# Kernel tuning notes

Hardware: AMD Instinct MI355X
Metric: run time of the kernel (lower is better)

The kernel has to match this reference:

```python
import jax, jax.numpy as jnp
import numpy as np
from jax import lax

B, S, IN, H = 16, 128, 200, 256


def _lstm_dir(x_tb, Wih, Whh, bih, bhh):
    # x_tb: [S, B, in]; PyTorch LSTM gate order (i, f, g, o)
    h0 = jnp.zeros((x_tb.shape[1], H), x_tb.dtype)

    def step(carry, x_t):
        h, c = carry
        g = x_t @ Wih.T + h @ Whh.T + bih + bhh  # [B, 4H]
        i, f, gg, o = jnp.split(g, 4, axis=-1)
        c = jax.nn.sigmoid(f) * c + jax.nn.sigmoid(i) * jnp.tanh(gg)
        h = jax.nn.sigmoid(o) * jnp.tanh(c)
        return (h, c), h

    _, hs = lax.scan(step, (h0, h0), x_tb)
    return hs  # [S, B, H]


def _bilstm_layer(x, Wih, Whh, bih, bhh):
    # x: [B, S, in]; params stacked over direction axis [2, ...]
    xt = jnp.swapaxes(x, 0, 1)
    f = _lstm_dir(xt, Wih[0], Whh[0], bih[0], bhh[0])
    b = _lstm_dir(xt[::-1], Wih[1], Whh[1], bih[1], bhh[1])[::-1]
    return jnp.swapaxes(jnp.concatenate([f, b], axis=-1), 0, 1)  # [B, S, 2H]


def _forward(sentence, Wih0, Whh0, bih0, bhh0, Wih1, Whh1, bih1, bhh1,
             W1, b1, W2, b2, W3, b3, tree):
    emb = _bilstm_layer(sentence, Wih0, Whh0, bih0, bhh0)  # [B,S,512]
    emb = _bilstm_layer(emb, Wih1, Whh1, bih1, bhh1)       # [B,S,512]
    D = emb.shape[-1]
    # fc1 on concat(emb[v1], emb[v2]) == per-node halves + broadcast add
    Ha = emb @ W1[:, :D].T   # [B,S,256] head part
    Hb = emb @ W1[:, D:].T   # [B,S,256] dependent part
    h1 = jax.nn.relu(Ha[:, :, None, :] + Hb[:, None, :, :] + b1)  # [B,S,S,256]
    h2 = jax.nn.relu(h1 @ W2.T + b2)                               # [B,S,S,128]
    score = jax.nn.relu(jnp.squeeze(h2 @ W3.T + b3, -1))           # [B,S,S]
    v = jnp.arange(S)
    # valid edges: dep >= 1, head != dep (root col 0 and diagonal stay 0)
    mask = (v[None, :] != v[:, None]) & (v[None, :] >= 1)
    score = score * mask[None, :, :]

    heads, deps = tree[:, 1:, 0], tree[:, 1:, 1]  # [B, S-1]
    K = S - 1
    idx = jnp.broadcast_to(deps[:, None, :], (B, S, K))
    cols = jnp.take_along_axis(score, idx, axis=2)     # score[b, j, dep_k]
    excl = v[None, :, None] == deps[:, None, :]        # exclude j == dep
    norm = jnp.sum(jnp.where(excl, 0.0, jnp.exp(cols)), axis=1)  # [B,K]
    num = score[jnp.arange(B)[:, None], heads, deps]             # [B,K]
    loss = jnp.sum(jnp.sum(jnp.log(norm) - num, axis=-1) / (S - 1))
    return loss, score


def setup_inputs() -> dict:
    key = jax.random.key(0)
    ks = jax.random.split(key, 17)
    sc = jnp.float32(0.05)

    def n(k, shape):
        return jax.random.normal(k, shape, jnp.float32) * sc

    return {
        "sentence": jax.random.normal(ks[0], (B, S, IN), jnp.float32),
        "Wih0": n(ks[1], (2, 4 * H, IN)),
        "Whh0": n(ks[2], (2, 4 * H, H)),
        "bih0": n(ks[3], (2, 4 * H)),
        "bhh0": n(ks[4], (2, 4 * H)),
        "Wih1": n(ks[5], (2, 4 * H, 2 * H)),
        "Whh1": n(ks[6], (2, 4 * H, H)),
        "bih1": n(ks[7], (2, 4 * H)),
        "bhh1": n(ks[8], (2, 4 * H)),
        "W1": n(ks[9], (256, 1024)),
        "b1": n(ks[10], (256,)),
        "W2": n(ks[11], (128, 256)),
        "b2": n(ks[12], (128,)),
        "W3": n(ks[13], (1, 128)),
        "b3": n(ks[14], (1,)),
        "real_dependency_tree": jax.random.randint(ks[15], (B, S, 2), 0, S, jnp.int32),
        "real_seq_len": jnp.full((B,), S, jnp.int32),
    }


def reference(sentence, Wih0, Whh0, bih0, bhh0, Wih1, Whh1, bih1, bhh1,
              W1, b1, W2, b2, W3, b3, real_dependency_tree, real_seq_len):
    # all sentences are full length S (real_seq_len == S), so shapes are static
    del real_seq_len
    return _forward(sentence, Wih0, Whh0, bih0, bhh0, Wih1, Whh1, bih1, bhh1,
                    W1, b1, W2, b2, W3, b3, real_dependency_tree)
```

## Files before the change

kernel.cpp:

```cpp
#include <hip/hip_runtime.h>
#include <hip/hip_bf16.h>
#include <cstdint>
#include <cstddef>


typedef __attribute__((ext_vector_type(8))) short bf16x8;
typedef __attribute__((ext_vector_type(4))) float f32x4;
typedef __attribute__((ext_vector_type(4))) unsigned short u16x4;

__device__ __forceinline__ float bf2f(unsigned short u) {
    return __uint_as_float(((unsigned)u) << 16);
}
__device__ __forceinline__ unsigned short f2bf(float f) {
    unsigned u = __float_as_uint(f);
    u = (u + 0x7FFFu + ((u >> 16) & 1u)) >> 16;
    return (unsigned short)u;
}

__device__ __forceinline__ unsigned f2e4m3(float f) {
    unsigned u = __float_as_uint(f);
    unsigned s = (u >> 24) & 0x80u;
    int expf_ = (int)((u >> 23) & 0xFF);
    if (expf_ == 0) return s;
    int exp = expf_ - 127;
    if (exp < -10) return s;
    unsigned M = (u & 0x7FFFFF) | 0x800000;
    int e8 = exp + 7;
    int shift = 20;
    if (e8 < 1) { shift = 21 - e8; e8 = 0; }
    unsigned q = M >> shift;
    unsigned rem = M & ((1u << shift) - 1u);
    unsigned half = 1u << (shift - 1);
    if (rem > half || (rem == half && (q & 1))) q++;
    if (q >= 16) { q >>= 1; e8++; }
    if (e8 == 0 && (q & 8)) e8 = 1;
    if (e8 >= 16 || (e8 == 15 && (q & 7) == 7)) return s | 0x7Eu;
    return s | ((unsigned)e8 << 4) | (q & 7u);
}


__global__ void k_transpose_N1024(const float* __restrict__ src, float* __restrict__ dst, int K) {
    int z = blockIdx.z;
    int idx = blockIdx.x * 256 + threadIdx.x;
    if (idx >= K * 1024) return;
    int k = idx >> 10, n = idx & 1023;
    dst[(size_t)z * K * 1024 + idx] = src[(size_t)z * 1024 * K + (size_t)n * K + k];
}

__global__ void k_wfrag8(const float* __restrict__ Whh, unsigned char* __restrict__ Wfrag8) {
    int idx = blockIdx.x * 256 + threadIdx.x;
    int l = idx & 63;
    int t = (idx >> 6) & 3;
    int ks = (idx >> 8) & 7;
    int w = (idx >> 11) & 15;
    int d = idx >> 15;
    int r = l & 15;
    int kbase = ks * 32 + (l >> 4) * 8;
    int row = (r & 3) * 256 + w * 16 + t * 4 + (r >> 2);
    const float* src = Whh + (size_t)d * (1024 * 256) + (size_t)row * 256 + kbase;
    unsigned char* dst = Wfrag8 + (size_t)idx * 8;
#pragma unroll
    for (int e = 0; e < 8; ++e) {
        int c = (e & 1) * 4 + (e >> 1);
        dst[e] = (unsigned char)f2e4m3(64.f * src[c]);
    }
}

__global__ void k_w2frag(const float* __restrict__ W2, unsigned short* __restrict__ w2f) {
    int idx = blockIdx.x * 256 + threadIdx.x;
    if (idx >= 4096) return;
    int l = idx & 63;
    int ks = (idx >> 6) & 7;
    int nt = idx >> 9;
    const float* src = W2 + (size_t)(nt * 16 + (l & 15)) * 256 + ks * 32 + (l >> 4) * 8;
    unsigned short* dst = w2f + (size_t)idx * 8;
#pragma unroll
    for (int e = 0; e < 8; ++e) dst[e] = f2bf(src[e]);
}

__global__ void k_w1t(const float* __restrict__ W1, float* __restrict__ dst) {
    int idx = blockIdx.x * 256 + threadIdx.x;
    if (idx >= 512 * 512) return;
    int k = idx >> 9, o = idx & 511;
    dst[idx] = (o < 256) ? W1[(size_t)o * 1024 + k] : W1[(size_t)(o - 256) * 1024 + 512 + k];
}

__global__ void k_bias(const float* __restrict__ bih0, const float* __restrict__ bhh0,
                       const float* __restrict__ bih1, const float* __restrict__ bhh1,
                       const float* __restrict__ b1,
                       float* __restrict__ bsum0, float* __restrict__ bsum1, float* __restrict__ bhab) {
    int idx = blockIdx.x * 256 + threadIdx.x;
    if (idx < 2048) bsum0[idx] = bih0[idx] + bhh0[idx];
    else if (idx < 4096) { int i = idx - 2048; bsum1[i] = bih1[i] + bhh1[i]; }
    else if (idx < 4608) { int i = idx - 4096; bhab[i] = (i < 256) ? b1[i] : 0.f; }
}

__global__ __launch_bounds__(256) void k_reorder(const float* __restrict__ xg, float* __restrict__ xgf) {
    int idx = blockIdx.x * 256 + threadIdx.x;
    int n4 = idx & 255;
    int m = (idx >> 8) & 2047;
    int d = idx >> 19;
    int n0 = n4 * 4;
    int q = n0 >> 8;
    int jbase = n0 & 255;
    int b = m >> 7, t = m & 127;
    float4 v = *(const float4*)(xg + ((size_t)(d * 2048 + m)) * 1024 + n0);
    float* base = xgf + (size_t)d * 2097152;
    float vv[4] = {v.x * 64.f, v.y * 64.f, v.z * 64.f, v.w * 64.f};
#pragma unroll
    for (int dj = 0; dj < 4; ++dj) {
        int j = jbase + dj;
        int fi = (t * 4096 + (j >> 4) * 256 + ((j >> 2) & 3) * 64 + dj * 16 + b) * 4 + q;
        base[fi] = vv[dj];
    }
}

__global__ __launch_bounds__(256) void k_gemm(
    const float* __restrict__ A, const float* __restrict__ Wt,
    const float* __restrict__ bias, float* __restrict__ out,
    int M, int K, int N)
{
    int z = blockIdx.z;
    const float* Wtz = Wt + (size_t)z * K * N;
    float* outz = out + (size_t)z * M * N;
    const float* biasz = bias + (size_t)z * N;

    __shared__ float As[16 * 512];
    int tid = threadIdx.x;
    int mq = tid >> 6;
    int nq = tid & 63;
    int n0 = blockIdx.x * 256 + nq * 4;
    int mbase = blockIdx.y * 16;

    for (int r = 0; r < 16; ++r) {
        const float* Ar = A + (size_t)(mbase + r) * K;
        for (int c = tid; c < K; c += 256) As[r * K + c] = Ar[c];
    }
    __syncthreads();

    float4 bv = *(const float4*)(biasz + n0);
    float acc[4][4];
#pragma unroll
    for (int mi = 0; mi < 4; mi++) { acc[mi][0] = bv.x; acc[mi][1] = bv.y; acc[mi][2] = bv.z; acc[mi][3] = bv.w; }

    const float* asr = As + (mq * 4) * K;
    for (int k = 0; k < K; ++k) {
        float4 w = *(const float4*)(Wtz + (size_t)k * N + n0);
        float x0 = asr[k];
        float x1 = asr[K + k];
        float x2 = asr[2 * K + k];
        float x3 = asr[3 * K + k];
        acc[0][0] += x0 * w.x; acc[0][1] += x0 * w.y; acc[0][2] += x0 * w.z; acc[0][3] += x0 * w.w;
        acc[1][0] += x1 * w.x; acc[1][1] += x1 * w.y; acc[1][2] += x1 * w.z; acc[1][3] += x1 * w.w;
        acc[2][0] += x2 * w.x; acc[2][1] += x2 * w.y; acc[2][2] += x2 * w.z; acc[2][3] += x2 * w.w;
        acc[3][0] += x3 * w.x; acc[3][1] += x3 * w.y; acc[3][2] += x3 * w.z; acc[3][3] += x3 * w.w;
    }
#pragma unroll
    for (int mi = 0; mi < 4; mi++) {
        size_t m = (size_t)mbase + mq * 4 + mi;
        *(float4*)(outz + m * N + n0) = make_float4(acc[mi][0], acc[mi][1], acc[mi][2], acc[mi][3]);
    }
}

__global__ __launch_bounds__(256) void k_gemm_tl(
    const unsigned short* __restrict__ embt, const float* __restrict__ Wt,
    const float* __restrict__ bias, float* __restrict__ out,
    int K, int N)
{
    int z = blockIdx.z;
    const float* Wtz = Wt + (size_t)z * K * N;
    float* outz = out + (size_t)z * 2048 * N;
    const float* biasz = bias + (size_t)z * N;

    __shared__ float As[16 * 512];
    int tid = threadIdx.x;
    int mq = tid >> 6;
    int nq = tid & 63;
    int n0 = blockIdx.x * 256 + nq * 4;
    int mbase = blockIdx.y * 16;
    int bb = mbase >> 7;
    int tt0 = mbase & 127;

    for (int r = 0; r < 16; ++r) {
        const unsigned short* Ar = embt + (size_t)(tt0 + r) * 8192 + bb;
        for (int c = tid; c < K; c += 256) As[r * K + c] = bf2f(Ar[c * 16]);
    }
    __syncthreads();

    float4 bv = *(const float4*)(biasz + n0);
    float acc[4][4];
#pragma unroll
    for (int mi = 0; mi < 4; mi++) { acc[mi][0] = bv.x; acc[mi][1] = bv.y; acc[mi][2] = bv.z; acc[mi][3] = bv.w; }

    const float* asr = As + (mq * 4) * K;
    for (int k = 0; k < K; ++k) {
        float4 w = *(const float4*)(Wtz + (size_t)k * N + n0);
        float x0 = asr[k];
        float x1 = asr[K + k];
        float x2 = asr[2 * K + k];
        float x3 = asr[3 * K + k];
        acc[0][0] += x0 * w.x; acc[0][1] += x0 * w.y; acc[0][2] += x0 * w.z; acc[0][3] += x0 * w.w;
        acc[1][0] += x1 * w.x; acc[1][1] += x1 * w.y; acc[1][2] += x1 * w.z; acc[1][3] += x1 * w.w;
        acc[2][0] += x2 * w.x; acc[2][1] += x2 * w.y; acc[2][2] += x2 * w.z; acc[2][3] += x2 * w.w;
        acc[3][0] += x3 * w.x; acc[3][1] += x3 * w.y; acc[3][2] += x3 * w.z; acc[3][3] += x3 * w.w;
    }
#pragma unroll
    for (int mi = 0; mi < 4; mi++) {
        size_t m = (size_t)mbase + mq * 4 + mi;
        *(float4*)(outz + m * N + n0) = make_float4(acc[mi][0], acc[mi][1], acc[mi][2], acc[mi][3]);
    }
}

#define GATE8(A, C, H) { \
    float gi = A[0] * 0.015625f, gf = A[1] * 0.015625f, gg = A[2] * 0.015625f, go = A[3] * 0.015625f; \
    float si = __builtin_amdgcn_rcpf(1.f + __expf(-gi)); \
    float sf = __builtin_amdgcn_rcpf(1.f + __expf(-gf)); \
    float so = __builtin_amdgcn_rcpf(1.f + __expf(-go)); \
    float eg = __expf(2.f * gg); \
    float tg = 1.f - 2.f * __builtin_amdgcn_rcpf(eg + 1.f); \
    C = sf * C + si * tg; \
    float ec = __expf(2.f * C); \
    float tc = 1.f - 2.f * __builtin_amdgcn_rcpf(ec + 1.f); \
    H = so * tc; }

__global__ __launch_bounds__(1024) void k_lstm_mfma(
    const float* __restrict__ xgf,
    const unsigned char* __restrict__ Wfrag8,
    unsigned short* __restrict__ embt)
{
    const int d = blockIdx.x;
    const int tid = threadIdx.x;
    const int w = tid >> 6;
    const int l = tid & 63;
    const int b = l & 15;
    const int jh = l >> 4;

    __shared__ __align__(16) unsigned char Wlds[131072];
    __shared__ __align__(8) unsigned char hB[4096];

    {
        const uint4* wsrc = (const uint4*)(Wfrag8 + (size_t)d * 262144);
        uint4* wdst = (uint4*)Wlds;
        for (int i = tid; i < 8192; i += 1024) wdst[i] = wsrc[i];
    }
    ((unsigned*)hB)[tid] = 0u;

    const int sgn = d ? -1 : 1;
    int t = d ? 127 : 0;
    const f32x4* xb = (const f32x4*)(xgf) + (size_t)d * 524288;
    const int xo = w * 256 + l;

    f32x4 a0 = xb[t * 4096 + xo];
    f32x4 a1 = xb[t * 4096 + xo + 64];
    f32x4 a2 = xb[t * 4096 + xo + 128];
    f32x4 a3 = xb[t * 4096 + xo + 192];

    float c0 = 0.f, c1 = 0.f, c2 = 0.f, c3 = 0.f;
    const int hrd = jh * 128 + b * 8;
    const unsigned char* Wp = Wlds + (size_t)w * 16384 + (size_t)l * 8;
    unsigned short* embp = embt + (size_t)d * 4096 + (size_t)w * 256 + l;
    unsigned char* hw = hB + w * 256 + b * 8 + jh * 2;
    __syncthreads();

    for (int s = 0; s < 128; ++s) {
#pragma unroll
        for (int ks = 0; ks < 8; ++ks) {
            long hf = *(const long*)(hB + ks * 512 + hrd);
            long w0 = *(const long*)(Wp + (ks * 4 + 0) * 512);
            long w1 = *(const long*)(Wp + (ks * 4 + 1) * 512);
            long w2 = *(const long*)(Wp + (ks * 4 + 2) * 512);
            long w3 = *(const long*)(Wp + (ks * 4 + 3) * 512);
            a0 = __builtin_amdgcn_mfma_f32_16x16x32_fp8_fp8(w0, hf, a0, 0, 0, 0);
            a1 = __builtin_amdgcn_mfma_f32_16x16x32_fp8_fp8(w1, hf, a1, 0, 0, 0);
            a2 = __builtin_amdgcn_mfma_f32_16x16x32_fp8_fp8(w2, hf, a2, 0, 0, 0);
            a3 = __builtin_amdgcn_mfma_f32_16x16x32_fp8_fp8(w3, hf, a3, 0, 0, 0);
        }

        float h0, h1, h2, h3;
        GATE8(a0, c0, h0);
        GATE8(a1, c1, h1);
        GATE8(a2, c2, h2);
        GATE8(a3, c3, h3);

        unsigned r01, r23;
        asm("v_cvt_pk_bf16_f32 %0, %1, %2" : "=v"(r01) : "v"(h0), "v"(h1));
        asm("v_cvt_pk_bf16_f32 %0, %1, %2" : "=v"(r23) : "v"(h2), "v"(h3));
        {
            unsigned short* p0 = embp + (size_t)t * 8192;
            p0[0]   = (unsigned short)r01;
            p0[64]  = (unsigned short)(r01 >> 16);
            p0[128] = (unsigned short)r23;
            p0[192] = (unsigned short)(r23 >> 16);
        }

        unsigned q01 = __builtin_amdgcn_cvt_pk_fp8_f32(h0, h1, 0, false);
        unsigned q23 = __builtin_amdgcn_cvt_pk_fp8_f32(h2, h3, 0, false);

        int tn = (s == 127) ? t : (t + sgn);
        a0 = xb[tn * 4096 + xo];
        a1 = xb[tn * 4096 + xo + 64];
        a2 = xb[tn * 4096 + xo + 128];
        a3 = xb[tn * 4096 + xo + 192];
        __syncthreads();
        *(unsigned short*)(hw)       = (unsigned short)q01;
        *(unsigned short*)(hw + 128) = (unsigned short)q23;
        __syncthreads();
        t = tn;
    }
}

__global__ __launch_bounds__(256, 2) void k_scorer_mfma(
    const float* __restrict__ HaHb, const unsigned short* __restrict__ w2f,
    const float* __restrict__ b2, const float* __restrict__ W3,
    const float* __restrict__ b3v, float* __restrict__ score)
{
    const int jt = blockIdx.x, it = blockIdx.y, b = blockIdx.z;
    const int j0 = jt * 16, i0 = it * 16;
    const int tid = threadIdx.x;
    const int w = tid >> 6;
    const int l = tid & 63;
    const int n_l = l & 15;
    const int kq = l >> 4;

    __shared__ __align__(16) unsigned short HaS[16 * 264];
    __shared__ __align__(16) unsigned short HbS[16 * 264];

    {
        const float* base = HaHb + ((size_t)(b * 128)) * 512;
        int rr = tid >> 4;
        int q = tid & 15;
#pragma unroll
        for (int rep = 0; rep < 4; ++rep) {
            int k0 = q * 4 + rep * 64;
            float4 va = *(const float4*)(base + (size_t)(i0 + rr) * 512 + k0);
            float4 vb = *(const float4*)(base + (size_t)(j0 + rr) * 512 + 256 + k0);
            u16x4 ua = { f2bf(va.x), f2bf(va.y), f2bf(va.z), f2bf(va.w) };
            u16x4 ub = { f2bf(vb.x), f2bf(vb.y), f2bf(vb.z), f2bf(vb.w) };
            *(u16x4*)(&HaS[rr * 264 + k0]) = ua;
            *(u16x4*)(&HbS[rr * 264 + k0]) = ub;
        }
    }

    float b2v[8], w3v[8];
#pragma unroll
    for (int nt = 0; nt < 8; ++nt) {
        b2v[nt] = b2[nt * 16 + n_l];
        w3v[nt] = W3[nt * 16 + n_l];
    }

    f32x4 acc[4][8];
#pragma unroll
    for (int il = 0; il < 4; ++il)
#pragma unroll
        for (int nt = 0; nt < 8; ++nt) acc[il][nt] = f32x4{0.f, 0.f, 0.f, 0.f};

    const bf16x8* wbase = (const bf16x8*)w2f;
    bf16x8 wf[8], wfn[8];
#pragma unroll
    for (int nt = 0; nt < 8; ++nt) wf[nt] = wbase[(nt * 8 + 0) * 64 + l];

    __syncthreads();

#pragma unroll
    for (int ks = 0; ks < 8; ++ks) {
        if (ks < 7) {
#pragma unroll
            for (int nt = 0; nt < 8; ++nt) wfn[nt] = wbase[(nt * 8 + ks + 1) * 64 + l];
        }
#pragma unroll
        for (int il = 0; il < 4; ++il) {
            const int irow = w * 4 + il;
            bf16x8 ha = *(const bf16x8*)(&HaS[irow * 264 + ks * 32 + kq * 8]);
            bf16x8 hb = *(const bf16x8*)(&HbS[n_l * 264 + ks * 32 + kq * 8]);
            bf16x8 av;
#pragma unroll
            for (int e = 0; e < 8; ++e) {
                float v = bf2f((unsigned short)ha[e]) + bf2f((unsigned short)hb[e]);
                v = v > 0.f ? v : 0.f;
                av[e] = (short)f2bf(v);
            }
#pragma unroll
            for (int nt = 0; nt < 8; ++nt)
                acc[il][nt] = __builtin_amdgcn_mfma_f32_16x16x32_bf16(av, wf[nt], acc[il][nt], 0, 0, 0);
        }
#pragma unroll
        for (int nt = 0; nt < 8; ++nt) wf[nt] = wfn[nt];
    }

    const float bb3 = b3v[0];
#pragma unroll
    for (int il = 0; il < 4; ++il) {
        float p[4];
#pragma unroll
        for (int reg = 0; reg < 4; ++reg) {
            float v = 0.f;
#pragma unroll
            for (int nt = 0; nt < 8; ++nt) {
                float h2v = acc[il][nt][reg] + b2v[nt];
                h2v = h2v > 0.f ? h2v : 0.f;
                v += h2v * w3v[nt];
            }
            p[reg] = v;
        }
#pragma unroll
        for (int m = 1; m < 16; m <<= 1) {
            p[0] += __shfl_xor(p[0], m);
            p[1] += __shfl_xor(p[1], m);
            p[2] += __shfl_xor(p[2], m);
            p[3] += __shfl_xor(p[3], m);
        }
        if (n_l == 0) {
            const int i = i0 + w * 4 + il;
            const int jb = j0 + kq * 4;
            float4 sv;
            float* pv = &sv.x;
#pragma unroll
            for (int reg = 0; reg < 4; ++reg) {
                int jg = jb + reg;
                float sc = p[reg] + bb3;
                sc = sc > 0.f ? sc : 0.f;
                if (jg == i || jg == 0) sc = 0.f;
                pv[reg] = sc;
            }
            *(float4*)(&score[((size_t)(b * 128 + i)) * 128 + jb]) = sv;
        }
    }
}

__global__ __launch_bounds__(128) void k_loss1(
    const float* __restrict__ score, const int* __restrict__ tree, float* __restrict__ res)
{
    int k = blockIdx.x;
    int b = blockIdx.y;
    int head = tree[((size_t)b * 128 + k + 1) * 2 + 0];
    int dep  = tree[((size_t)b * 128 + k + 1) * 2 + 1];
    int i = threadIdx.x;
    float s = score[((size_t)b * 128 + i) * 128 + dep];
    float v = (i == dep) ? 0.f : __expf(s);
    __shared__ float redu[2];
#pragma unroll
    for (int off = 32; off >= 1; off >>= 1) v += __shfl_down(v, off, 64);
    if ((i & 63) == 0) redu[i >> 6] = v;
    __syncthreads();
    if (i == 0) {
        float norm = redu[0] + redu[1];
        float num = score[((size_t)b * 128 + head) * 128 + dep];
        res[b * 127 + k] = __logf(norm) - num;
    }
}

__global__ __launch_bounds__(256) void k_loss2(const float* __restrict__ res, float* __restrict__ out) {
    int tid = threadIdx.x;
    float a = 0.f;
    for (int idx = tid; idx < 16 * 127; idx += 256) a += res[idx];
    __shared__ float sm[256];
    sm[tid] = a;
    __syncthreads();
    for (int off = 128; off >= 1; off >>= 1) {
        if (tid < off) sm[tid] += sm[tid + off];
        __syncthreads();
    }
    if (tid == 0) out[0] = sm[0] / 127.f;
}

extern "C" void kernel_launch(void* const* d_in, const int* in_sizes, int n_in,
                              void* d_out, int out_size, void* d_ws, size_t ws_size,
                              hipStream_t stream) {
    (void)in_sizes; (void)n_in; (void)out_size; (void)ws_size;
    const float* X    = (const float*)d_in[0];
    const float* Wih0 = (const float*)d_in[1];
    const float* Whh0 = (const float*)d_in[2];
    const float* bih0 = (const float*)d_in[3];
    const float* bhh0 = (const float*)d_in[4];
    const float* Wih1 = (const float*)d_in[5];
    const float* Whh1 = (const float*)d_in[6];
    const float* bih1 = (const float*)d_in[7];
    const float* bhh1 = (const float*)d_in[8];
    const float* W1   = (const float*)d_in[9];
    const float* b1   = (const float*)d_in[10];
    const float* W2   = (const float*)d_in[11];
    const float* b2   = (const float*)d_in[12];
    const float* W3   = (const float*)d_in[13];
    const float* b3   = (const float*)d_in[14];
    const int*   tree = (const int*)d_in[15];
    float* out = (float*)d_out;

    float* ws = (float*)d_ws;
    size_t o = 0;
    float* WihT0 = ws + o; o += (size_t)2 * 200 * 1024;
    float* WihT1 = ws + o; o += (size_t)2 * 512 * 1024;
    float* W1T   = ws + o; o += (size_t)512 * 512;
    float* bsum0 = ws + o; o += 2048;
    float* bsum1 = ws + o; o += 2048;
    float* bhab  = ws + o; o += 512;
    unsigned char* Wf0 = (unsigned char*)(ws + o); o += (size_t)2 * 16 * 8 * 4 * 64 * 8 / 4;
    unsigned char* Wf1 = (unsigned char*)(ws + o); o += (size_t)2 * 16 * 8 * 4 * 64 * 8 / 4;
    unsigned short* w2f = (unsigned short*)(ws + o); o += (size_t)8 * 8 * 64 * 8 / 2;
    float* xg   = ws + o; o += (size_t)2 * 2048 * 1024;
    float* xgf  = ws + o; o += (size_t)2 * 2048 * 1024;
    unsigned short* embt0 = (unsigned short*)(ws + o); o += (size_t)128 * 512 * 16 / 2;
    unsigned short* embt1 = (unsigned short*)(ws + o); o += (size_t)128 * 512 * 16 / 2;
    float* HaHb = ws + o; o += (size_t)2048 * 512;
    float* res  = ws + o; o += 2048;

    k_transpose_N1024<<<dim3(800, 1, 2), 256, 0, stream>>>(Wih0, WihT0, 200);
    k_transpose_N1024<<<dim3(2048, 1, 2), 256, 0, stream>>>(Wih1, WihT1, 512);
    k_wfrag8<<<256, 256, 0, stream>>>(Whh0, Wf0);
    k_wfrag8<<<256, 256, 0, stream>>>(Whh1, Wf1);
    k_w2frag<<<16, 256, 0, stream>>>(W2, w2f);
    k_w1t<<<1024, 256, 0, stream>>>(W1, W1T);
    k_bias<<<18, 256, 0, stream>>>(bih0, bhh0, bih1, bhh1, b1, bsum0, bsum1, bhab);

    k_gemm<<<dim3(4, 128, 2), 256, 0, stream>>>(X, WihT0, bsum0, xg, 2048, 200, 1024);
    k_reorder<<<4096, 256, 0, stream>>>(xg, xgf);
    k_lstm_mfma<<<2, 1024, 0, stream>>>(xgf, Wf0, embt0);
    k_gemm_tl<<<dim3(4, 128, 2), 256, 0, stream>>>(embt0, WihT1, bsum1, xg, 512, 1024);
    k_reorder<<<4096, 256, 0, stream>>>(xg, xgf);
    k_lstm_mfma<<<2, 1024, 0, stream>>>(xgf, Wf1, embt1);
    k_gemm_tl<<<dim3(2, 128, 1), 256, 0, stream>>>(embt1, W1T, bhab, HaHb, 512, 512);
    k_scorer_mfma<<<dim3(8, 8, 16), 256, 0, stream>>>(HaHb, w2f, b2, W3, b3, out + 1);
    k_loss1<<<dim3(127, 16), 128, 0, stream>>>(out + 1, tree, res);
    k_loss2<<<1, 256, 0, stream>>>(res, out);
}
```

Baseline: 796.2 us.

## Interleave fp8 Whh fragments for 128-bit loads and split weights between LDS and global

The pre-packed fp8 recurrent weight fragments are reordered so each lane's four tile fragments for a k-step are contiguous 32 bytes. The recurrent loop can then fetch them with two 16-byte loads instead of four 8-byte loads. Waves 0-7 read weights from LDS, while waves 8-15 read their weights directly from global memory (L2/L1) each step. This is meant to cut LDS instruction count and bandwidth pressure on the serial LSTM critical path, but the global-reading waves risk higher per-step latency, and the LDS staging may be inconsistent with the new layout.

Result: slower. 1.064 ms (+33.7%).

```diff
diff --git a/kernel.cpp b/kernel.cpp
--- a/kernel.cpp
+++ b/kernel.cpp
@@ -7,6 +7,7 @@
 typedef __attribute__((ext_vector_type(8))) short bf16x8;
 typedef __attribute__((ext_vector_type(4))) float f32x4;
 typedef __attribute__((ext_vector_type(4))) unsigned short u16x4;
+typedef __attribute__((ext_vector_type(2))) long i64x2;
 
 __device__ __forceinline__ float bf2f(unsigned short u) {
     return __uint_as_float(((unsigned)u) << 16);
@@ -49,16 +50,16 @@
 
 __global__ void k_wfrag8(const float* __restrict__ Whh, unsigned char* __restrict__ Wfrag8) {
     int idx = blockIdx.x * 256 + threadIdx.x;
-    int l = idx & 63;
-    int t = (idx >> 6) & 3;
+    int t4 = idx & 3;
+    int l = (idx >> 2) & 63;
     int ks = (idx >> 8) & 7;
     int w = (idx >> 11) & 15;
     int d = idx >> 15;
     int r = l & 15;
     int kbase = ks * 32 + (l >> 4) * 8;
-    int row = (r & 3) * 256 + w * 16 + t * 4 + (r >> 2);
+    int row = (r & 3) * 256 + w * 16 + t4 * 4 + (r >> 2);
     const float* src = Whh + (size_t)d * (1024 * 256) + (size_t)row * 256 + kbase;
-    unsigned char* dst = Wfrag8 + (size_t)idx * 8;
+    unsigned char* dst = Wfrag8 + ((size_t)(((d * 16 + w) * 8 + ks) * 64 + l)) * 32 + t4 * 8;
 #pragma unroll
     for (int e = 0; e < 8; ++e) {
         int c = (e & 1) * 4 + (e >> 1);
@@ -257,23 +258,35 @@
 
     float c0 = 0.f, c1 = 0.f, c2 = 0.f, c3 = 0.f;
     const int hrd = jh * 128 + b * 8;
-    const unsigned char* Wp = Wlds + (size_t)w * 16384 + (size_t)l * 8;
+    const unsigned char* WpL = Wlds + (size_t)w * 16384 + (size_t)l * 32;
+    const unsigned char* WpG = Wfrag8 + (size_t)d * 262144 + (size_t)w * 16384 + (size_t)l * 32;
     unsigned short* embp = embt + (size_t)d * 4096 + (size_t)w * 256 + l;
     unsigned char* hw = hB + w * 256 + b * 8 + jh * 2;
     __syncthreads();
 
     for (int s = 0; s < 128; ++s) {
-#pragma unroll
-        for (int ks = 0; ks < 8; ++ks) {
-            long hf = *(const long*)(hB + ks * 512 + hrd);
-            long w0 = *(const long*)(Wp + (ks * 4 + 0) * 512);
-            long w1 = *(const long*)(Wp + (ks * 4 + 1) * 512);
-            long w2 = *(const long*)(Wp + (ks * 4 + 2) * 512);
-            long w3 = *(const long*)(Wp + (ks * 4 + 3) * 512);
-            a0 = __builtin_amdgcn_mfma_f32_16x16x32_fp8_fp8(w0, hf, a0, 0, 0, 0);
-            a1 = __builtin_amdgcn_mfma_f32_16x16x32_fp8_fp8(w1, hf, a1, 0, 0, 0);
-            a2 = __builtin_amdgcn_mfma_f32_16x16x32_fp8_fp8(w2, hf, a2, 0, 0, 0);
-            a3 = __builtin_amdgcn_mfma_f32_16x16x32_fp8_fp8(w3, hf, a3, 0, 0, 0);
+        if (w < 8) {
+#pragma unroll
+            for (int ks = 0; ks < 8; ++ks) {
+                long hf = *(const long*)(hB + ks * 512 + hrd);
+                i64x2 pa = *(const i64x2*)(WpL + ks * 2048);
+                i64x2 pb = *(const i64x2*)(WpL + ks * 2048 + 16);
+                a0 = __builtin_amdgcn_mfma_f32_16x16x32_fp8_fp8(pa.x, hf, a0, 0, 0, 0);
+                a1 = __builtin_amdgcn_mfma_f32_16x16x32_fp8_fp8(pa.y, hf, a1, 0, 0, 0);
+                a2 = __builtin_amdgcn_mfma_f32_16x16x32_fp8_fp8(pb.x, hf, a2, 0, 0, 0);
+                a3 = __builtin_amdgcn_mfma_f32_16x16x32_fp8_fp8(pb.y, hf, a3, 0, 0, 0);
+            }
+        } else {
+#pragma unroll
+            for (int ks = 0; ks < 8; ++ks) {
+                long hf = *(const long*)(hB + ks * 512 + hrd);
+                i64x2 pa = *(const i64x2*)(WpG + ks * 2048);
+                i64x2 pb = *(const i64x2*)(WpG + ks * 2048 + 16);
+                a0 = __builtin_amdgcn_mfma_f32_16x16x32_fp8_fp8(pa.x, hf, a0, 0, 0, 0);
+                a1 = __builtin_amdgcn_mfma_f32_16x16x32_fp8_fp8(pa.y, hf, a1, 0, 0, 0);
+                a2 = __builtin_amdgcn_mfma_f32_16x16x32_fp8_fp8(pb.x, hf, a2, 0, 0, 0);
+                a3 = __builtin_amdgcn_mfma_f32_16x16x32_fp8_fp8(pb.y, hf, a3, 0, 0, 0);
+            }
         }
 
         float h0, h1, h2, h3;
```

## Split each LSTM direction across two co-located CUs with flag-based h exchange

Applied to the files above, without the earlier changes.

Each LSTM direction now runs on two 512-thread workgroups instead of one 1024-thread workgroup. Sixteen blocks are launched, each reads its XCC id, and pairs that share an XCC are picked so that two pairs do the work while the rest exit. Half of each block's recurrent weights is held in registers and the other half in LDS. Every timestep the two halves of the hidden state are swapped through a global payload buffer using release/acquire flags. This spreads per-step MFMA and LDS traffic over two CUs, but adds an inter-CU round trip through L2 on every step, bounded spin loops that could hang or desync, and two extra memsets.

After: 916.6 us. +15.1%, slower.

```diff
diff --git a/kernel.cpp b/kernel.cpp
--- a/kernel.cpp
+++ b/kernel.cpp
@@ -223,32 +223,89 @@
     float tc = 1.f - 2.f * __builtin_amdgcn_rcpf(ec + 1.f); \
     H = so * tc; }
 
-__global__ __launch_bounds__(1024) void k_lstm_mfma(
+__global__ __launch_bounds__(512, 2) void k_lstm_mfma(
     const float* __restrict__ xgf,
     const unsigned char* __restrict__ Wfrag8,
-    unsigned short* __restrict__ embt)
+    unsigned short* __restrict__ embt,
+    int* ctrl,
+    unsigned char* pay)
 {
-    const int d = blockIdx.x;
+    const int bid = blockIdx.x;
     const int tid = threadIdx.x;
-    const int w = tid >> 6;
+    const int wv = tid >> 6;
     const int l = tid & 63;
     const int b = l & 15;
     const int jh = l >> 4;
 
-    __shared__ __align__(16) unsigned char Wlds[131072];
+    __shared__ __align__(16) unsigned char Wlds[81920];
     __shared__ __align__(8) unsigned char hB[4096];
-
+    __shared__ int role_sh[4];
+
+    if (tid == 0) {
+        unsigned xcc = 0;
+        asm volatile("s_getreg_b32 %0, hwreg(20, 0, 32)" : "=s"(xcc));
+        __hip_atomic_store(&ctrl[1 + bid], (int)(xcc & 7), __ATOMIC_RELAXED, __HIP_MEMORY_SCOPE_AGENT);
+        __hip_atomic_fetch_add(&ctrl[0], 1, __ATOMIC_ACQ_REL, __HIP_MEMORY_SCOPE_AGENT);
+        long it = 0;
+        while (__hip_atomic_load(&ctrl[0], __ATOMIC_ACQUIRE, __HIP_MEMORY_SCOPE_AGENT) < 16 && it < (1 << 24)) {
+            ++it; __builtin_amdgcn_s_sleep(2);
+        }
+        int x[16];
+        for (int i = 0; i < 16; ++i)
+            x[i] = __hip_atomic_load(&ctrl[1 + i], __ATOMIC_RELAXED, __HIP_MEMORY_SCOPE_AGENT) & 7;
+        int pend[8];
+        for (int i = 0; i < 8; ++i) pend[i] = -1;
+        int np = 0, dd = -1, hh = 0;
+        for (int i = 0; i < 16; ++i) {
+            int xc = x[i];
+            if (pend[xc] < 0) pend[xc] = i;
+            else {
+                if (np < 2) {
+                    if (pend[xc] == bid) { dd = np; hh = 0; }
+                    else if (i == bid) { dd = np; hh = 1; }
+                }
+                np++;
+                pend[xc] = -1;
+            }
+        }
+        if (np < 2) {
+            dd = (bid < 4) ? (bid >> 1) : -1;
+            hh = bid & 1;
+        }
+        role_sh[0] = dd; role_sh[1] = hh;
+    }
+    __syncthreads();
+    const int d = role_sh[0];
+    const int hh = role_sh[1];
+    if (d < 0) return;
+
+    const int sg = hh * 8 + wv;
     {
-        const uint4* wsrc = (const uint4*)(Wfrag8 + (size_t)d * 262144);
+        const uint4* wsrc = (const uint4*)(Wfrag8 + (size_t)d * 262144 + (size_t)(hh * 8 + 4) * 16384);
         uint4* wdst = (uint4*)Wlds;
-        for (int i = tid; i < 8192; i += 1024) wdst[i] = wsrc[i];
-    }
-    ((unsigned*)hB)[tid] = 0u;
+        for (int i = tid; i < 4096; i += 512) wdst[i] = wsrc[i];
+    }
+    ((uint64_t*)hB)[tid] = 0ull;
+
+    long W0[8][4];
+    if (wv < 4) {
+        const unsigned char* wg0 = Wfrag8 + ((size_t)(d * 16 + sg)) * 16384;
+#pragma unroll
+        for (int ks = 0; ks < 8; ++ks)
+#pragma unroll
+            for (int t4 = 0; t4 < 4; ++t4)
+                W0[ks][t4] = *(const long*)(wg0 + ((size_t)((ks * 4 + t4) * 64 + l)) * 8);
+#pragma unroll
+        for (int ks = 0; ks < 8; ++ks)
+#pragma unroll
+            for (int t4 = 0; t4 < 4; ++t4)
+                asm volatile("" : "+v"(W0[ks][t4]));
+    }
 
     const int sgn = d ? -1 : 1;
     int t = d ? 127 : 0;
     const f32x4* xb = (const f32x4*)(xgf) + (size_t)d * 524288;
-    const int xo = w * 256 + l;
+    const int xo = sg * 256 + l;
 
     f32x4 a0 = xb[t * 4096 + xo];
     f32x4 a1 = xb[t * 4096 + xo + 64];
@@ -257,23 +314,36 @@
 
     float c0 = 0.f, c1 = 0.f, c2 = 0.f, c3 = 0.f;
     const int hrd = jh * 128 + b * 8;
-    const unsigned char* Wp = Wlds + (size_t)w * 16384 + (size_t)l * 8;
-    unsigned short* embp = embt + (size_t)d * 4096 + (size_t)w * 256 + l;
-    unsigned char* hw = hB + w * 256 + b * 8 + jh * 2;
+    const unsigned char* WpL = Wlds + (size_t)(wv - 4) * 16384 + (size_t)l * 8;
+    unsigned short* embp = embt + (size_t)d * 4096 + (size_t)sg * 256 + l;
+    unsigned char* hw = hB + sg * 256 + b * 8 + jh * 2;
+    int* myflag = &ctrl[16 + d * 2 + hh];
+    int* pflag  = &ctrl[16 + d * 2 + (1 - hh)];
     __syncthreads();
 
     for (int s = 0; s < 128; ++s) {
-#pragma unroll
-        for (int ks = 0; ks < 8; ++ks) {
-            long hf = *(const long*)(hB + ks * 512 + hrd);
-            long w0 = *(const long*)(Wp + (ks * 4 + 0) * 512);
-            long w1 = *(const long*)(Wp + (ks * 4 + 1) * 512);
-            long w2 = *(const long*)(Wp + (ks * 4 + 2) * 512);
-            long w3 = *(const long*)(Wp + (ks * 4 + 3) * 512);
-            a0 = __builtin_amdgcn_mfma_f32_16x16x32_fp8_fp8(w0, hf, a0, 0, 0, 0);
-            a1 = __builtin_amdgcn_mfma_f32_16x16x32_fp8_fp8(w1, hf, a1, 0, 0, 0);
-            a2 = __builtin_amdgcn_mfma_f32_16x16x32_fp8_fp8(w2, hf, a2, 0, 0, 0);
-            a3 = __builtin_amdgcn_mfma_f32_16x16x32_fp8_fp8(w3, hf, a3, 0, 0, 0);
+        if (wv < 4) {
+#pragma unroll
+            for (int ks = 0; ks < 8; ++ks) {
+                long hf = *(const long*)(hB + ks * 512 + hrd);
+                a0 = __builtin_amdgcn_mfma_f32_16x16x32_fp8_fp8(W0[ks][0], hf, a0, 0, 0, 0);
+                a1 = __builtin_amdgcn_mfma_f32_16x16x32_fp8_fp8(W0[ks][1], hf, a1, 0, 0, 0);
+                a2 = __builtin_amdgcn_mfma_f32_16x16x32_fp8_fp8(W0[ks][2], hf, a2, 0, 0, 0);
+                a3 = __builtin_amdgcn_mfma_f32_16x16x32_fp8_fp8(W0[ks][3], hf, a3, 0, 0, 0);
+            }
+        } else {
+#pragma unroll
+            for (int ks = 0; ks < 8; ++ks) {
+                long hf = *(const long*)(hB + ks * 512 + hrd);
+                long w0 = *(const long*)(WpL + (ks * 4 + 0) * 512);
+                long w1 = *(const long*)(WpL + (ks * 4 + 1) * 512);
+                long w2 = *(const long*)(WpL + (ks * 4 + 2) * 512);
+                long w3 = *(const long*)(WpL + (ks * 4 + 3) * 512);
+                a0 = __builtin_amdgcn_mfma_f32_16x16x32_fp8_fp8(w0, hf, a0, 0, 0, 0);
+                a1 = __builtin_amdgcn_mfma_f32_16x16x32_fp8_fp8(w1, hf, a1, 0, 0, 0);
+                a2 = __builtin_amdgcn_mfma_f32_16x16x32_fp8_fp8(w2, hf, a2, 0, 0, 0);
+                a3 = __builtin_amdgcn_mfma_f32_16x16x32_fp8_fp8(w3, hf, a3, 0, 0, 0);
+            }
         }
 
         float h0, h1, h2, h3;
@@ -292,20 +362,42 @@
             p0[128] = (unsigned short)r23;
             p0[192] = (unsigned short)(r23 >> 16);
         }
-
         unsigned q01 = __builtin_amdgcn_cvt_pk_fp8_f32(h0, h1, 0, false);
         unsigned q23 = __builtin_amdgcn_cvt_pk_fp8_f32(h2, h3, 0, false);
 
-        int tn = (s == 127) ? t : (t + sgn);
-        a0 = xb[tn * 4096 + xo];
-        a1 = xb[tn * 4096 + xo + 64];
-        a2 = xb[tn * 4096 + xo + 128];
-        a3 = xb[tn * 4096 + xo + 192];
-        __syncthreads();
-        *(unsigned short*)(hw)       = (unsigned short)q01;
-        *(unsigned short*)(hw + 128) = (unsigned short)q23;
-        __syncthreads();
-        t = tn;
+        if (s < 127) {
+            unsigned char* pw = pay + (((size_t)(d * 2 + hh)) * 2 + (s & 1)) * 2048 + wv * 256 + b * 8 + jh * 2;
+            *(unsigned short*)(pw)       = (unsigned short)q01;
+            *(unsigned short*)(pw + 128) = (unsigned short)q23;
+            asm volatile("s_waitcnt vmcnt(0)" ::: "memory");
+            __syncthreads();
+
+            *(unsigned short*)(hw)       = (unsigned short)q01;
+            *(unsigned short*)(hw + 128) = (unsigned short)q23;
+
+            if (tid == 0) {
+                __hip_atomic_store(myflag, s + 1, __ATOMIC_RELEASE, __HIP_MEMORY_SCOPE_AGENT);
+                int it = 0;
+                while (__hip_atomic_load(pflag, __ATOMIC_RELAXED, __HIP_MEMORY_SCOPE_AGENT) <= s && it < (1 << 16)) {
+                    ++it; __builtin_amdgcn_s_sleep(1);
+                }
+                (void)__hip_atomic_load(pflag, __ATOMIC_ACQUIRE, __HIP_MEMORY_SCOPE_AGENT);
+            }
+            __syncthreads();
+
+            {
+                const unsigned* pr = (const unsigned*)(pay + (((size_t)(d * 2 + (1 - hh))) * 2 + (s & 1)) * 2048);
+                unsigned v = __hip_atomic_load(&pr[tid], __ATOMIC_RELAXED, __HIP_MEMORY_SCOPE_AGENT);
+                *(unsigned*)(hB + (size_t)(1 - hh) * 2048 + tid * 4) = v;
+            }
+            int tn = t + sgn;
+            a0 = xb[tn * 4096 + xo];
+            a1 = xb[tn * 4096 + xo + 64];
+            a2 = xb[tn * 4096 + xo + 128];
+            a3 = xb[tn * 4096 + xo + 192];
+            __syncthreads();
+            t = tn;
+        }
     }
 }
 
@@ -502,6 +594,8 @@
     unsigned short* embt1 = (unsigned short*)(ws + o); o += (size_t)128 * 512 * 16 / 2;
     float* HaHb = ws + o; o += (size_t)2048 * 512;
     float* res  = ws + o; o += 2048;
+    int* ctrl = (int*)(ws + o); o += 32;
+    unsigned char* pay = (unsigned char*)(ws + o); o += 4096;
 
     k_transpose_N1024<<<dim3(800, 1, 2), 256, 0, stream>>>(Wih0, WihT0, 200);
     k_transpose_N1024<<<dim3(2048, 1, 2), 256, 0, stream>>>(Wih1, WihT1, 512);
@@ -513,10 +607,12 @@
 
     k_gemm<<<dim3(4, 128, 2), 256, 0, stream>>>(X, WihT0, bsum0, xg, 2048, 200, 1024);
     k_reorder<<<4096, 256, 0, stream>>>(xg, xgf);
-    k_lstm_mfma<<<2, 1024, 0, stream>>>(xgf, Wf0, embt0);
+    hipMemsetAsync(ctrl, 0, 128, stream);
+    k_lstm_mfma<<<16, 512, 0, stream>>>(xgf, Wf0, embt0, ctrl, pay);
     k_gemm_tl<<<dim3(4, 128, 2), 256, 0, stream>>>(embt0, WihT1, bsum1, xg, 512, 1024);
     k_reorder<<<4096, 256, 0, stream>>>(xg, xgf);
-    k_lstm_mfma<<<2, 1024, 0, stream>>>(xgf, Wf1, embt1);
+    hipMemsetAsync(ctrl, 0, 128, stream);
+    k_lstm_mfma<<<16, 512, 0, stream>>>(xgf, Wf1, embt1, ctrl, pay);
     k_gemm_tl<<<dim3(2, 128, 1), 256, 0, stream>>>(embt1, W1T, bhab, HaHb, 512, 512);
     k_scorer_mfma<<<dim3(8, 8, 16), 256, 0, stream>>>(HaHb, w2f, b2, W3, b3, out + 1);
     k_loss1<<<dim3(127, 16), 128, 0, stream>>>(out + 1, tree, res);
```
